# Performance work log

Hardware: AMD Instinct MI355X
Metric: run time of the kernel (lower is better)

Reference implementation:

```python
import jax, jax.numpy as jnp
import numpy as np

KH, KW = 3, 3
K_TERMS = KH * KW + 1  # ones (linear/bias) + 9 shifted patches
# pair indices (i<=j), same ordering as the original layer
_PAIRS = [(i, j) for i in range(K_TERMS) for j in range(i, K_TERMS)]
II = np.array([p[0] for p in _PAIRS])  # [55]
JJ = np.array([p[1] for p in _PAIRS])  # [55]


def setup_inputs() -> dict:
    key = jax.random.key(0)
    k1, k2 = jax.random.split(key)
    B, H, W, C, O = 8, 56, 56, 64, 128
    inputs = jax.random.normal(k1, (B, H, W, C), dtype=jnp.float32)
    # glorot-ish scale for the [1,1,55,C,O] conv3d kernel (squeezed to [55,C,O])
    fan = 55 * C + O
    kernel = jax.random.normal(k2, (55, C, O), dtype=jnp.float32) * jnp.sqrt(2.0 / fan)
    return {"inputs": inputs, "kernel": kernel}


def reference(inputs, kernel):
    B, H, W, C = inputs.shape
    # 'same' padding for stride 1: pad_total = k - 1, asymmetric split as in TF
    ph, pw = KH - 1, KW - 1
    xp = jnp.pad(inputs, ((0, 0), (ph // 2, ph - ph // 2), (pw // 2, pw - pw // 2), (0, 0)))
    # im2col-style shifted slices, row-major over (r, c) like i//kw, i%kw
    shifts = jnp.stack(
        [xp[:, r:r + H, c:c + W, :] for r in range(KH) for c in range(KW)],
        axis=3,
    )  # [B,H,W,9,C]
    ones = jnp.ones((B, H, W, 1, C), dtype=inputs.dtype)
    S = jnp.concatenate([ones, shifts], axis=3)  # [B,H,W,10,C]
    # pairwise quadratic features (includes bias = ones*ones and linear = ones*shift)
    quad = S[:, :, :, II, :] * S[:, :, :, JJ, :]  # [B,H,W,55,C]
    # 1x1x1 conv3d over depth-55 == contraction over (pair, channel)
    return jnp.einsum('bhwpc,pco->bhwo', quad, kernel)  # [B,H,W,O]
```

## Files before the change

### kernel.cpp

```cpp
#include <hip/hip_runtime.h>


#define CB 8
#define CH 56
#define CW 56
#define CC 64
#define CO 128
#define RS 72

typedef __attribute__((ext_vector_type(8))) _Float16 v8hf;
typedef __attribute__((ext_vector_type(16))) float f16f;
typedef __attribute__((address_space(3))) const _Float16 lds_cf16;

__device__ constexpr int PII[55] = {0,0,0,0,0,0,0,0,0,0, 1,1,1,1,1,1,1,1,1, 2,2,2,2,2,2,2,2,
                                    3,3,3,3,3,3,3, 4,4,4,4,4,4, 5,5,5,5,5, 6,6,6,6, 7,7,7, 8,8, 9};
__device__ constexpr int PJJ[55] = {0,1,2,3,4,5,6,7,8,9, 1,2,3,4,5,6,7,8,9, 2,3,4,5,6,7,8,9,
                                    3,4,5,6,7,8,9, 4,5,6,7,8,9, 5,6,7,8,9, 6,7,8,9, 7,8,9, 8,9, 9};

__global__ __launch_bounds__(256) void prep_kernel(const float* __restrict__ K,
                                                   _Float16* __restrict__ BtF) {
  __shared__ float tile[CC * CO];
  const int p = blockIdx.x;
  const int t = threadIdx.x;
  const float* src = K + (size_t)p * CC * CO;
#pragma unroll
  for (int e = 0; e < 8; ++e) {
    const int idx = t * 4 + e * 1024;
    *(float4*)&tile[idx] = *(const float4*)&src[idx];
  }
  __syncthreads();
#pragma unroll
  for (int e4 = 0; e4 < 4; ++e4) {
    const int idx = e4 * 256 + t;
    const int lane = idx & 63;
    const int nqq = (idx >> 6) & 3;
    const int ksq = idx >> 8;
    const int n = nqq * 32 + (lane & 31);
    const int kb = ksq * 16 + (lane >> 5) * 8;
    _Float16 ov[8];
#pragma unroll
    for (int e = 0; e < 8; ++e)
      ov[e] = (_Float16)tile[(kb + e) * CO + n];
    *(v8hf*)(BtF + ((size_t)p * 1024 + idx) * 8) = *(const v8hf*)ov;
  }
}

__global__ __launch_bounds__(256, 1) void quad_kernel(const float* __restrict__ in,
                                                      const _Float16* __restrict__ BtF,
                                                      float* __restrict__ out) {
  __shared__ _Float16 rowsH[4][64][RS];

  const int t = threadIdx.x;
  const int b = blockIdx.x / (CH / 2);
  const int h0 = (blockIdx.x % (CH / 2)) * 2;

  {
    const int col = t >> 2;
    const int cg = (t & 3) * 16;
    const int w = col - 1;
#pragma unroll
    for (int r = 0; r < 4; ++r) {
      const int hh = h0 + r - 1;
      const bool valid = (hh >= 0) && (hh < CH) && (w >= 0) && (w < CW);
      float4 v0 = make_float4(0.f, 0.f, 0.f, 0.f), v1 = v0, v2 = v0, v3 = v0;
      if (valid) {
        const float* s = in + (((size_t)(b * CH + hh)) * CW + w) * CC + cg;
        v0 = *(const float4*)(s);
        v1 = *(const float4*)(s + 4);
        v2 = *(const float4*)(s + 8);
        v3 = *(const float4*)(s + 12);
      }
      _Float16 pv[16];
      pv[0] = (_Float16)v0.x;  pv[1] = (_Float16)v0.y;  pv[2] = (_Float16)v0.z;  pv[3] = (_Float16)v0.w;
      pv[4] = (_Float16)v1.x;  pv[5] = (_Float16)v1.y;  pv[6] = (_Float16)v1.z;  pv[7] = (_Float16)v1.w;
      pv[8] = (_Float16)v2.x;  pv[9] = (_Float16)v2.y;  pv[10] = (_Float16)v2.z; pv[11] = (_Float16)v2.w;
      pv[12] = (_Float16)v3.x; pv[13] = (_Float16)v3.y; pv[14] = (_Float16)v3.z; pv[15] = (_Float16)v3.w;
      _Float16* d = &rowsH[r][col][cg];
      *(v8hf*)(d) = *(const v8hf*)&pv[0];
      *(v8hf*)(d + 8) = *(const v8hf*)&pv[8];
    }
  }

  const int lane = t & 63;
  const int nq = t >> 6;
  const int ml = lane & 31;
  const int hk = lane >> 5;
  const int h8 = hk * 8;

  f16f acc00, acc01, acc10, acc11;
#pragma unroll
  for (int r = 0; r < 16; ++r) { acc00[r] = 0.f; acc01[r] = 0.f; acc10[r] = 0.f; acc11[r] = 0.f; }

  const _Float16* Bw = BtF + (size_t)(nq * 64 + lane) * 8;
  const v8hf vone = {1, 1, 1, 1, 1, 1, 1, 1};

  lds_cf16* lds3 = (lds_cf16*)&rowsH[0][0][0];

  v8hf ring[11];
#pragma unroll
  for (int p = 0; p < 11; ++p) {
    const _Float16* ba = Bw + (size_t)p * 8192;
    asm volatile("global_load_dwordx4 %0, %1, off" : "=v"(ring[p]) : "v"(ba));
  }

  __syncthreads();

#pragma unroll 1
  for (int ks = 0; ks < 4; ++ks) {
    const int koff = ks * 16 + h8;
    v8hf sv0[12], sv1[12];
#pragma unroll
    for (int rr = 0; rr < 4; ++rr)
#pragma unroll
      for (int dx = 0; dx < 3; ++dx) {
        const int c0 = ml + dx;
        int c1 = 32 + ml + dx; c1 = c1 > 63 ? 63 : c1;
        lds_cf16* p0 = lds3 + (rr * 64 + c0) * RS + koff;
        lds_cf16* p1 = lds3 + (rr * 64 + c1) * RS + koff;
        asm volatile("ds_read_b128 %0, %1" : "=v"(sv0[rr * 3 + dx]) : "v"(p0));
        asm volatile("ds_read_b128 %0, %1" : "=v"(sv1[rr * 3 + dx]) : "v"(p1));
      }
    asm volatile("s_waitcnt lgkmcnt(0)"
                 : "+v"(sv0[0]), "+v"(sv0[1]), "+v"(sv0[2]), "+v"(sv0[3]),
                   "+v"(sv0[4]), "+v"(sv0[5]), "+v"(sv0[6]), "+v"(sv0[7]),
                   "+v"(sv0[8]), "+v"(sv0[9]), "+v"(sv0[10]), "+v"(sv0[11]),
                   "+v"(sv1[0]), "+v"(sv1[1]), "+v"(sv1[2]), "+v"(sv1[3]),
                   "+v"(sv1[4]), "+v"(sv1[5]), "+v"(sv1[6]), "+v"(sv1[7]),
                   "+v"(sv1[8]), "+v"(sv1[9]), "+v"(sv1[10]), "+v"(sv1[11]));

    const int ksn = (ks < 3) ? ks + 1 : 3;
#pragma unroll
    for (int p = 0; p < 55; ++p) {
      asm volatile("s_waitcnt vmcnt(10)" : "+v"(ring[p % 11]));
      const v8hf bb = ring[p % 11];
      {
        const int p2 = (p < 44) ? p + 11 : p - 44;
        const int ks2 = (p < 44) ? ks : ksn;
        const _Float16* ba = Bw + (size_t)p2 * 8192 + ks2 * 2048;
        asm volatile("global_load_dwordx4 %0, %1, off" : "=v"(ring[p % 11]) : "v"(ba));
      }
      const int pi = PII[p], pj = PJJ[p];
      v8hf a00, a01, a10, a11;
      if (pi == 0) {
        if (pj == 0) { a00 = vone; a01 = vone; a10 = vone; a11 = vone; }
        else {
          const int dy = (pj - 1) / 3, dx = (pj - 1) % 3;
          a00 = sv0[dy * 3 + dx];        a01 = sv1[dy * 3 + dx];
          a10 = sv0[(dy + 1) * 3 + dx];  a11 = sv1[(dy + 1) * 3 + dx];
        }
      } else {
        const int dyi = (pi - 1) / 3, dxi = (pi - 1) % 3;
        const int dyj = (pj - 1) / 3, dxj = (pj - 1) % 3;
        a00 = sv0[dyi * 3 + dxi] * sv0[dyj * 3 + dxj];
        a01 = sv1[dyi * 3 + dxi] * sv1[dyj * 3 + dxj];
        a10 = sv0[(dyi + 1) * 3 + dxi] * sv0[(dyj + 1) * 3 + dxj];
        a11 = sv1[(dyi + 1) * 3 + dxi] * sv1[(dyj + 1) * 3 + dxj];
      }
      acc00 = __builtin_amdgcn_mfma_f32_32x32x16_f16(a00, bb, acc00, 0, 0, 0);
      acc01 = __builtin_amdgcn_mfma_f32_32x32x16_f16(a01, bb, acc01, 0, 0, 0);
      acc10 = __builtin_amdgcn_mfma_f32_32x32x16_f16(a10, bb, acc10, 0, 0, 0);
      acc11 = __builtin_amdgcn_mfma_f32_32x32x16_f16(a11, bb, acc11, 0, 0, 0);
    }
  }
  asm volatile("s_waitcnt vmcnt(0)");

#pragma unroll
  for (int rw = 0; rw < 2; ++rw) {
    float* ob = out + ((size_t)(b * CH + h0 + rw) * CW) * CO + nq * 32 + ml;
    const f16f accc0 = rw ? acc10 : acc00;
    const f16f accc1 = rw ? acc11 : acc01;
#pragma unroll
    for (int r = 0; r < 16; ++r) {
      const int wp = (r & 3) + 8 * (r >> 2) + 4 * hk;
      ob[(size_t)wp * CO] = accc0[r];
    }
#pragma unroll
    for (int r = 0; r < 12; ++r) {
      const int wp = 32 + (r & 3) + 8 * (r >> 2) + 4 * hk;
      ob[(size_t)wp * CO] = accc1[r];
    }
  }
}

extern "C" void kernel_launch(void* const* d_in, const int* in_sizes, int n_in,
                              void* d_out, int out_size, void* d_ws, size_t ws_size,
                              hipStream_t stream) {
  const float* in = (const float*)d_in[0];
  const float* K = (const float*)d_in[1];
  float* out = (float*)d_out;
  _Float16* BtF = (_Float16*)d_ws;
  (void)in_sizes; (void)n_in; (void)out_size; (void)ws_size;

  prep_kernel<<<55, 256, 0, stream>>>(K, BtF);
  quad_kernel<<<CB * (CH / 2), 256, 0, stream>>>(in, BtF, out);
}
```

Measured before the change: 86.18 us.

## Split K dimension across two wave groups with LDS reduction

```diff
diff --git a/kernel.cpp b/kernel.cpp
--- a/kernel.cpp
+++ b/kernel.cpp
@@ -9,6 +9,7 @@
 #define RS 72
 
 typedef __attribute__((ext_vector_type(8))) _Float16 v8hf;
+typedef __attribute__((ext_vector_type(4))) float f4;
 typedef __attribute__((ext_vector_type(16))) float f16f;
 typedef __attribute__((address_space(3))) const _Float16 lds_cf16;
 
@@ -45,21 +46,27 @@
   }
 }
 
-__global__ __launch_bounds__(256, 1) void quad_kernel(const float* __restrict__ in,
-                                                      const _Float16* __restrict__ BtF,
-                                                      float* __restrict__ out) {
+__global__
+__attribute__((amdgpu_flat_work_group_size(512, 512), amdgpu_waves_per_eu(2)))
+void quad_kernel(const float* __restrict__ in,
+                 const _Float16* __restrict__ BtF,
+                 float* __restrict__ out) {
   __shared__ _Float16 rowsH[4][64][RS];
+  __shared__ float red[4 * 4 * 64 * 16];
 
   const int t = threadIdx.x;
   const int b = blockIdx.x / (CH / 2);
   const int h0 = (blockIdx.x % (CH / 2)) * 2;
 
   {
-    const int col = t >> 2;
-    const int cg = (t & 3) * 16;
+    const int tt = t & 255;
+    const int r0 = t >> 8;
+    const int col = tt >> 2;
+    const int cg = (tt & 3) * 16;
     const int w = col - 1;
 #pragma unroll
-    for (int r = 0; r < 4; ++r) {
+    for (int rx = 0; rx < 2; ++rx) {
+      const int r = r0 + rx * 2;
       const int hh = h0 + r - 1;
       const bool valid = (hh >= 0) && (hh < CH) && (w >= 0) && (w < CW);
       float4 v0 = make_float4(0.f, 0.f, 0.f, 0.f), v1 = v0, v2 = v0, v3 = v0;
@@ -82,7 +89,9 @@
   }
 
   const int lane = t & 63;
-  const int nq = t >> 6;
+  const int wid = t >> 6;
+  const int khalf = wid >> 2;
+  const int nq = wid & 3;
   const int ml = lane & 31;
   const int hk = lane >> 5;
   const int h8 = hk * 8;
@@ -91,14 +100,14 @@
 #pragma unroll
   for (int r = 0; r < 16; ++r) { acc00[r] = 0.f; acc01[r] = 0.f; acc10[r] = 0.f; acc11[r] = 0.f; }
 
-  const _Float16* Bw = BtF + (size_t)(nq * 64 + lane) * 8;
+  const _Float16* Bw = BtF + (size_t)(nq * 64 + lane) * 8 + (size_t)khalf * 4096;
   const v8hf vone = {1, 1, 1, 1, 1, 1, 1, 1};
 
   lds_cf16* lds3 = (lds_cf16*)&rowsH[0][0][0];
 
-  v8hf ring[11];
-#pragma unroll
-  for (int p = 0; p < 11; ++p) {
+  v8hf ring[5];
+#pragma unroll
+  for (int p = 0; p < 5; ++p) {
     const _Float16* ba = Bw + (size_t)p * 8192;
     asm volatile("global_load_dwordx4 %0, %1, off" : "=v"(ring[p]) : "v"(ba));
   }
@@ -106,8 +115,8 @@
   __syncthreads();
 
 #pragma unroll 1
-  for (int ks = 0; ks < 4; ++ks) {
-    const int koff = ks * 16 + h8;
+  for (int ksl = 0; ksl < 2; ++ksl) {
+    const int koff = (khalf * 2 + ksl) * 16 + h8;
     v8hf sv0[12], sv1[12];
 #pragma unroll
     for (int rr = 0; rr < 4; ++rr)
@@ -128,16 +137,15 @@
                    "+v"(sv1[4]), "+v"(sv1[5]), "+v"(sv1[6]), "+v"(sv1[7]),
                    "+v"(sv1[8]), "+v"(sv1[9]), "+v"(sv1[10]), "+v"(sv1[11]));
 
-    const int ksn = (ks < 3) ? ks + 1 : 3;
 #pragma unroll
     for (int p = 0; p < 55; ++p) {
-      asm volatile("s_waitcnt vmcnt(10)" : "+v"(ring[p % 11]));
-      const v8hf bb = ring[p % 11];
+      asm volatile("s_waitcnt vmcnt(4)" : "+v"(ring[p % 5]));
+      const v8hf bb = ring[p % 5];
       {
-        const int p2 = (p < 44) ? p + 11 : p - 44;
-        const int ks2 = (p < 44) ? ks : ksn;
-        const _Float16* ba = Bw + (size_t)p2 * 8192 + ks2 * 2048;
-        asm volatile("global_load_dwordx4 %0, %1, off" : "=v"(ring[p % 11]) : "v"(ba));
+        const int s2 = (ksl * 55 + p + 5) % 110;
+        const int ksl2 = s2 / 55, p2 = s2 % 55;
+        const _Float16* ba = Bw + (size_t)p2 * 8192 + ksl2 * 2048;
+        asm volatile("global_load_dwordx4 %0, %1, off" : "=v"(ring[p % 5]) : "v"(ba));
       }
       const int pi = PII[p], pj = PJJ[p];
       v8hf a00, a01, a10, a11;
@@ -164,20 +172,43 @@
   }
   asm volatile("s_waitcnt vmcnt(0)");
 
-#pragma unroll
-  for (int rw = 0; rw < 2; ++rw) {
-    float* ob = out + ((size_t)(b * CH + h0 + rw) * CW) * CO + nq * 32 + ml;
-    const f16f accc0 = rw ? acc10 : acc00;
-    const f16f accc1 = rw ? acc11 : acc01;
-#pragma unroll
-    for (int r = 0; r < 16; ++r) {
-      const int wp = (r & 3) + 8 * (r >> 2) + 4 * hk;
-      ob[(size_t)wp * CO] = accc0[r];
-    }
-#pragma unroll
-    for (int r = 0; r < 12; ++r) {
-      const int wp = 32 + (r & 3) + 8 * (r >> 2) + 4 * hk;
-      ob[(size_t)wp * CO] = accc1[r];
+  if (khalf) {
+#pragma unroll
+    for (int tl = 0; tl < 4; ++tl) {
+      const f16f& a = tl == 0 ? acc00 : tl == 1 ? acc01 : tl == 2 ? acc10 : acc11;
+      float* rb = &red[((nq * 4 + tl) * 64 + lane) * 16];
+#pragma unroll
+      for (int g = 0; g < 4; ++g)
+        *(f4*)(rb + g * 4) = (f4){a[g * 4 + 0], a[g * 4 + 1], a[g * 4 + 2], a[g * 4 + 3]};
+    }
+  }
+  __syncthreads();
+  if (!khalf) {
+#pragma unroll
+    for (int tl = 0; tl < 4; ++tl) {
+      f16f& a = tl == 0 ? acc00 : tl == 1 ? acc01 : tl == 2 ? acc10 : acc11;
+      const float* rb = &red[((nq * 4 + tl) * 64 + lane) * 16];
+#pragma unroll
+      for (int g = 0; g < 4; ++g) {
+        const f4 v = *(const f4*)(rb + g * 4);
+        a[g * 4 + 0] += v[0]; a[g * 4 + 1] += v[1]; a[g * 4 + 2] += v[2]; a[g * 4 + 3] += v[3];
+      }
+    }
+#pragma unroll
+    for (int rw = 0; rw < 2; ++rw) {
+      float* ob = out + ((size_t)(b * CH + h0 + rw) * CW) * CO + nq * 32 + ml;
+      const f16f accc0 = rw ? acc10 : acc00;
+      const f16f accc1 = rw ? acc11 : acc01;
+#pragma unroll
+      for (int r = 0; r < 16; ++r) {
+        const int wp = (r & 3) + 8 * (r >> 2) + 4 * hk;
+        ob[(size_t)wp * CO] = accc0[r];
+      }
+#pragma unroll
+      for (int r = 0; r < 12; ++r) {
+        const int wp = 32 + (r & 3) + 8 * (r >> 2) + 4 * hk;
+        ob[(size_t)wp * CO] = accc1[r];
+      }
     }
   }
 }
@@ -192,5 +223,5 @@
   (void)in_sizes; (void)n_in; (void)out_size; (void)ws_size;
 
   prep_kernel<<<55, 256, 0, stream>>>(K, BtF);
-  quad_kernel<<<CB * (CH / 2), 256, 0, stream>>>(in, BtF, out);
+  quad_kernel<<<CB * (CH / 2), 512, 0, stream>>>(in, BtF, out);
 }
```

New measurement: 92.43 us. 7.3% more time.
